# Performance work log

Measured on AMD Instinct MI355X. Metric: run time of the kernel, lower is better.

Reference implementation:

```python
import jax, jax.numpy as jnp
import numpy as np

B, T, C = 4, 128, 512
NH, HS = 8, 64          # n_head, head_dim = C // NH
ORDER = 3               # attention_order
SCALE = 1.0 / np.sqrt(HS)


def setup_inputs() -> dict:
    key = jax.random.key(0)
    ks = jax.random.split(key, 7)
    s = 0.02
    return {
        "x": jax.random.normal(ks[0], (B, T, C), jnp.float32),
        "Wp0": jax.random.normal(ks[1], (C, C), jnp.float32) * s,
        "Wp1": jax.random.normal(ks[2], (C, C), jnp.float32) * s,
        "Wp2": jax.random.normal(ks[3], (C, C), jnp.float32) * s,
        "Wv0": jax.random.normal(ks[4], (HS, HS), jnp.float32) * s,
        "Wv1": jax.random.normal(ks[5], (HS, HS), jnp.float32) * s,
        "Wc": jax.random.normal(ks[6], (C, C), jnp.float32) * s,
    }


def _heads(x, W):
    # Linear then split heads: (B,T,C) -> (B,NH,T,HS)
    return (x @ W).reshape(B, T, NH, HS).transpose(0, 2, 1, 3)


def _causal_mask(t, order):
    # indices grid [T]^order, True where i0 >= i1 >= ... >= i_{order-1}
    idx = jnp.arange(t)
    g = jnp.stack(jnp.meshgrid(*([idx] * order), indexing='ij'), axis=-1)
    return jnp.all(jnp.diff(g, axis=-1) <= 0, axis=-1)


def reference(x, Wp0, Wp1, Wp2, Wv0, Wv1, Wc):
    p0 = _heads(x, Wp0)  # (B,NH,T,HS)
    p1 = _heads(x, Wp1)
    p2 = _heads(x, Wp2)

    # pairwise scores, then higher-order broadcast exactly as the torch einsum
    # ('bh...i,bhkd->bh...ik' sums the key over d and broadcasts — faithful).
    att = jnp.einsum('bhid,bhjd->bhij', p0, p1) * SCALE        # (B,NH,T,T)
    att = jnp.einsum('bh...i,bhkd->bh...ik', att, p2)          # (B,NH,T,T,T)

    mask = _causal_mask(T, ORDER)[None, None]                  # (1,1,T,T,T)
    att = jnp.where(mask, att, -jnp.inf)
    att = jax.nn.softmax(att.reshape(B, NH, T, T * T), axis=-1)

    # value tensors with broadcasted elementwise product over the order dims
    V0 = (p1 @ Wv0)[:, :, :, None, :]   # (B,NH,T,1,HS)
    V1 = (p2 @ Wv1)[:, :, None, :, :]   # (B,NH,1,T,HS)
    V = (V0 * V1).reshape(B, NH, T * T, HS)

    y = jnp.einsum('bhij,bhjd->bhid', att, V)                  # (B,NH,T,HS)
    y = y.transpose(0, 2, 1, 3).reshape(B, T, C)
    return y @ Wc
```

## Files before the change

kernel.cpp:

```cpp
#include <hip/hip_runtime.h>
#include <hip/hip_bf16.h>
#include <math.h>

#define B 4
#define T 128
#define C 512
#define NH 8
#define HS 64
#define BH (B*NH)

typedef __attribute__((ext_vector_type(8))) short bf16x8;
typedef __attribute__((ext_vector_type(4))) float f32x4;

__device__ __forceinline__ unsigned short bfc(float x) {
    return __builtin_bit_cast(unsigned short, __float2bfloat16(x));
}
__device__ __forceinline__ unsigned int pk_bf16(float a, float b) {
    return (unsigned int)bfc(a) | ((unsigned int)bfc(b) << 16);
}
__device__ __forceinline__ float lo_f(unsigned int g) {
    return __builtin_bit_cast(float, g << 16);
}
__device__ __forceinline__ float hi_f(unsigned int g) {
    return __builtin_bit_cast(float, g & 0xffff0000u);
}

__global__ __launch_bounds__(256) void proj_kernel(
    const float* __restrict__ X,
    const float* __restrict__ Wp0, const float* __restrict__ Wp1, const float* __restrict__ Wp2,
    unsigned short* __restrict__ p0b, unsigned short* __restrict__ p1b,
    unsigned short* __restrict__ p2b, float* __restrict__ rr)
{
    __shared__ __align__(16) unsigned short As[32][72];
    __shared__ __align__(16) unsigned short Bs[64][72];
    __shared__ float Ls[64][69];
    __shared__ float sRS[4][32];
    const int z = blockIdx.z;
    const float* W = (z == 0) ? Wp0 : (z == 1) ? Wp1 : Wp2;
    const int m0 = blockIdx.y * 32, n0 = blockIdx.x * 64;
    const int tid = threadIdx.x;
    const int w = tid >> 6, lane = tid & 63, quad = lane >> 4, l16 = lane & 15;
    f32x4 acc[2];
    #pragma unroll
    for (int mt = 0; mt < 2; ++mt) acc[mt] = (f32x4){0.f, 0.f, 0.f, 0.f};

    for (int k0 = 0; k0 < 512; k0 += 64) {
        __syncthreads();
        {
            const int row = tid >> 3, c8 = (tid & 7) * 8;
            const float4 a = *(const float4*)&X[(size_t)(m0 + row) * 512 + k0 + c8];
            const float4 b = *(const float4*)&X[(size_t)(m0 + row) * 512 + k0 + c8 + 4];
            uint4 o;
            o.x = pk_bf16(a.x, a.y);
            o.y = pk_bf16(a.z, a.w);
            o.z = pk_bf16(b.x, b.y);
            o.w = pk_bf16(b.z, b.w);
            *(uint4*)&As[row][c8] = o;
        }
        #pragma unroll
        for (int it = 0; it < 4; ++it) {
            const int q = tid + it * 256;
            const int row = q >> 4, c4 = (q & 15) * 4;
            const float4 v = *(const float4*)&W[(size_t)(k0 + row) * 512 + n0 + c4];
            Ls[row][c4 + 0] = v.x; Ls[row][c4 + 1] = v.y;
            Ls[row][c4 + 2] = v.z; Ls[row][c4 + 3] = v.w;
        }
        __syncthreads();
        #pragma unroll
        for (int it = 0; it < 2; ++it) {
            const int q = tid + it * 256;
            const int nrow = q >> 3, k8 = (q & 7) * 8;
            uint4 o;
            o.x = pk_bf16(Ls[k8 + 0][nrow], Ls[k8 + 1][nrow]);
            o.y = pk_bf16(Ls[k8 + 2][nrow], Ls[k8 + 3][nrow]);
            o.z = pk_bf16(Ls[k8 + 4][nrow], Ls[k8 + 5][nrow]);
            o.w = pk_bf16(Ls[k8 + 6][nrow], Ls[k8 + 7][nrow]);
            *(uint4*)&Bs[nrow][k8] = o;
        }
        __syncthreads();
        #pragma unroll
        for (int kt = 0; kt < 2; ++kt) {
            const bf16x8 b8 = *(const bf16x8*)&Bs[w * 16 + l16][kt * 32 + quad * 8];
            #pragma unroll
            for (int mt = 0; mt < 2; ++mt) {
                const bf16x8 a8 = *(const bf16x8*)&As[mt * 16 + l16][kt * 32 + quad * 8];
                acc[mt] = __builtin_amdgcn_mfma_f32_16x16x32_bf16(a8, b8, acc[mt], 0, 0, 0);
            }
        }
    }

    {
        const int n = n0 + w * 16 + l16;
        const int h = n >> 6, d = n & 63;
        unsigned short* pz = (z == 0) ? p0b : (z == 1) ? p1b : p2b;
        #pragma unroll
        for (int mt = 0; mt < 2; ++mt) {
            #pragma unroll
            for (int r = 0; r < 4; ++r) {
                const int m = m0 + mt * 16 + quad * 4 + r;
                const int bb = m >> 7, t = m & 127;
                pz[((size_t)(bb * NH + h) * T + t) * HS + d] = bfc(acc[mt][r]);
            }
        }
    }
    if (z == 2) {
        #pragma unroll
        for (int mt = 0; mt < 2; ++mt)
            #pragma unroll
            for (int r = 0; r < 4; ++r) {
                float v = acc[mt][r];
                v += __shfl_xor(v, 1, 64); v += __shfl_xor(v, 2, 64);
                v += __shfl_xor(v, 4, 64); v += __shfl_xor(v, 8, 64);
                if (l16 == 0) sRS[w][mt * 16 + quad * 4 + r] = v;
            }
        __syncthreads();
        if (tid < 32) {
            const float s = sRS[0][tid] + sRS[1][tid] + sRS[2][tid] + sRS[3][tid];
            const int m = m0 + tid, bb = m >> 7, tl = m & 127, h = n0 >> 6;
            rr[(bb * NH + h) * T + tl] = s;
        }
    }
}

__global__ __launch_bounds__(512, 4) void attn_kernel(
    const unsigned short* __restrict__ p0b, const unsigned short* __restrict__ p1b,
    const unsigned short* __restrict__ p2b, const float* __restrict__ rr,
    const float* __restrict__ Wv0, const float* __restrict__ Wv1,
    unsigned short* __restrict__ Yb)
{
    __shared__ __align__(16) unsigned short sV0T[64][136];
    __shared__ __align__(16) unsigned short sV1T[64][136];
    __shared__ __align__(16) union {
        unsigned short sWv[64][72];
        float sY[8][8][64];
    } u2;
    __shared__ float sS[8][128];
    __shared__ float srr[128];
    __shared__ float sZarr[8][8];

    const int bid = blockIdx.x;
    const int bh = bid & (BH - 1);
    const int ig = bid >> 5;
    const int tid = threadIdx.x;
    const int w = tid >> 6;
    const int lane = tid & 63;
    const int quad = lane >> 4;
    const int l16 = lane & 15;

    if (tid < 128) srr[tid] = rr[bh * T + tid];

    #pragma unroll
    for (int it = 0; it < 2; ++it) {
        const int k = (tid >> 4) + it * 32;
        const int d0 = (tid & 15) * 4;
        const float4 wv = *(const float4*)&Wv0[(size_t)k * 64 + d0];
        u2.sWv[d0 + 0][k] = bfc(wv.x); u2.sWv[d0 + 1][k] = bfc(wv.y);
        u2.sWv[d0 + 2][k] = bfc(wv.z); u2.sWv[d0 + 3][k] = bfc(wv.w);
    }
    __syncthreads();

    {
        f32x4 vacc[4];
        #pragma unroll
        for (int mt = 0; mt < 4; ++mt) vacc[mt] = (f32x4){0.f, 0.f, 0.f, 0.f};
        #pragma unroll
        for (int kt = 0; kt < 2; ++kt) {
            const bf16x8 b8 = *(const bf16x8*)&p1b[((size_t)bh * T + w * 16 + l16) * HS + kt * 32 + quad * 8];
            #pragma unroll
            for (int mt = 0; mt < 4; ++mt) {
                const bf16x8 a8 = *(const bf16x8*)&u2.sWv[mt * 16 + l16][kt * 32 + quad * 8];
                vacc[mt] = __builtin_amdgcn_mfma_f32_16x16x32_bf16(a8, b8, vacc[mt], 0, 0, 0);
            }
        }
        #pragma unroll
        for (int mt = 0; mt < 4; ++mt)
            #pragma unroll
            for (int r = 0; r < 4; ++r)
                sV0T[mt * 16 + quad * 4 + r][w * 16 + l16] = bfc(vacc[mt][r]);
    }
    __syncthreads();

    #pragma unroll
    for (int it = 0; it < 2; ++it) {
        const int k = (tid >> 4) + it * 32;
        const int d0 = (tid & 15) * 4;
        const float4 wv = *(const float4*)&Wv1[(size_t)k * 64 + d0];
        u2.sWv[d0 + 0][k] = bfc(wv.x); u2.sWv[d0 + 1][k] = bfc(wv.y);
        u2.sWv[d0 + 2][k] = bfc(wv.z); u2.sWv[d0 + 3][k] = bfc(wv.w);
    }
    __syncthreads();

    {
        f32x4 vacc[4];
        #pragma unroll
        for (int mt = 0; mt < 4; ++mt) vacc[mt] = (f32x4){0.f, 0.f, 0.f, 0.f};
        #pragma unroll
        for (int kt = 0; kt < 2; ++kt) {
            const bf16x8 b8 = *(const bf16x8*)&p2b[((size_t)bh * T + w * 16 + l16) * HS + kt * 32 + quad * 8];
            #pragma unroll
            for (int mt = 0; mt < 4; ++mt) {
                const bf16x8 a8 = *(const bf16x8*)&u2.sWv[mt * 16 + l16][kt * 32 + quad * 8];
                vacc[mt] = __builtin_amdgcn_mfma_f32_16x16x32_bf16(a8, b8, vacc[mt], 0, 0, 0);
            }
        }
        #pragma unroll
        for (int mt = 0; mt < 4; ++mt)
            #pragma unroll
            for (int r = 0; r < 4; ++r)
                sV1T[mt * 16 + quad * 4 + r][w * 16 + l16] = bfc(vacc[mt][r]);
    }
    __syncthreads();

    {
        const int qr = l16 & 7;
        const int irow = (qr & 1) ? (16 * qr + 15 - ig) : (16 * qr + ig);
        const unsigned short* ap = p0b + ((size_t)bh * T + irow) * HS + (quad << 3);
        const unsigned short* bp = p1b + (size_t)bh * T * HS + (quad << 3);
        f32x4 s0 = (f32x4){0.f, 0.f, 0.f, 0.f};
        #pragma unroll
        for (int kt = 0; kt < 2; ++kt) {
            const bf16x8 a8 = *(const bf16x8*)(ap + (kt << 5));
            const bf16x8 b0 = *(const bf16x8*)(bp + (size_t)((w << 4) + l16) * HS + (kt << 5));
            s0 = __builtin_amdgcn_mfma_f32_16x16x32_bf16(a8, b0, s0, 0, 0, 0);
        }
        if (quad < 2) {
            #pragma unroll
            for (int r = 0; r < 4; ++r)
                sS[quad * 4 + r][(w << 4) + l16] = s0[r] * 0.125f;
        }
    }
    #pragma unroll
    for (int it = 0; it < 8; ++it) ((float*)u2.sY)[tid + it * 512] = 0.f;
    if (tid < 64) ((float*)sZarr)[tid] = 0.f;
    __syncthreads();

    const float L2E = 1.4426950408889634f;

    float mhat;
    {
        float aS = 0.f;
        #pragma unroll
        for (int q = 0; q < 8; ++q) {
            aS = fmaxf(aS, fabsf(sS[q][lane]));
            aS = fmaxf(aS, fabsf(sS[q][64 + lane]));
        }
        float aR = fmaxf(fabsf(srr[lane]), fabsf(srr[64 + lane]));
        #pragma unroll
        for (int off = 32; off; off >>= 1) {
            aS = fmaxf(aS, __shfl_xor(aS, off, 64));
            aR = fmaxf(aR, __shfl_xor(aR, off, 64));
        }
        mhat = aS * aR;
    }
    const float bexp = -mhat * L2E;
    const int jrow = (w << 4) + l16;
    const int ktmax = w >> 1;

    for (int qq = 7; qq >= w; --qq) {
        const int i = (qq & 1) ? (16 * qq + 15 - ig) : (16 * qq + ig);
        const float aL = sS[qq][jrow] * L2E;
        const bool rowok = (jrow <= i);
        f32x4 acc[4];
        #pragma unroll
        for (int dt = 0; dt < 4; ++dt) acc[dt] = (f32x4){0.f, 0.f, 0.f, 0.f};
        float zacc = 0.f;

        for (int kt = 0; kt <= ktmax; ++kt) {
            const int kbase = (kt << 5) + (quad << 3);
            float rk[8];
            *(float4*)&rk[0] = *(const float4*)&srr[kbase];
            *(float4*)&rk[4] = *(const float4*)&srr[kbase + 4];
            const int dlim = rowok ? (jrow - kbase) : -1;
            float e[8];
            #pragma unroll
            for (int q = 0; q < 8; ++q) {
                const float ex = __builtin_amdgcn_exp2f(fmaf(aL, rk[q], bexp));
                e[q] = (q <= dlim) ? ex : 0.f;
                zacc += e[q];
            }
            uint4 o;
            o.x = pk_bf16(e[0], e[1]);
            o.y = pk_bf16(e[2], e[3]);
            o.z = pk_bf16(e[4], e[5]);
            o.w = pk_bf16(e[6], e[7]);
            const bf16x8 a8 = __builtin_bit_cast(bf16x8, o);
            #pragma unroll
            for (int dt = 0; dt < 4; ++dt) {
                const bf16x8 b8 = *(const bf16x8*)&sV1T[(dt << 4) + l16][(quad << 3) + (kt << 5)];
                acc[dt] = __builtin_amdgcn_mfma_f32_16x16x32_bf16(a8, b8, acc[dt], 0, 0, 0);
            }
        }

        float part[4];
        #pragma unroll
        for (int dt = 0; dt < 4; ++dt) {
            const uint2 uu = *(const uint2*)&sV0T[(dt << 4) + l16][(w << 4) + (quad << 2)];
            float p = 0.f;
            if (w < qq) {
                p = fmaf(lo_f(uu.x), acc[dt][0], p);
                p = fmaf(hi_f(uu.x), acc[dt][1], p);
                p = fmaf(lo_f(uu.y), acc[dt][2], p);
                p = fmaf(hi_f(uu.y), acc[dt][3], p);
            } else {
                const int jb = (w << 4) + (quad << 2);
                if (jb + 0 <= i) p = fmaf(lo_f(uu.x), acc[dt][0], p);
                if (jb + 1 <= i) p = fmaf(hi_f(uu.x), acc[dt][1], p);
                if (jb + 2 <= i) p = fmaf(lo_f(uu.y), acc[dt][2], p);
                if (jb + 3 <= i) p = fmaf(hi_f(uu.y), acc[dt][3], p);
            }
            p += __shfl_xor(p, 16, 64);
            p += __shfl_xor(p, 32, 64);
            part[dt] = p;
        }
        const float sel = (quad == 0) ? part[0] : (quad == 1) ? part[1] : (quad == 2) ? part[2] : part[3];
        u2.sY[qq][w][lane] = sel;

        #pragma unroll
        for (int off = 32; off; off >>= 1) zacc += __shfl_xor(zacc, off, 64);
        if (lane == 0) sZarr[qq][w] = zacc;
    }
    __syncthreads();

    {
        const int qq = w;
        const int i = (qq & 1) ? (16 * qq + 15 - ig) : (16 * qq + ig);
        float Z = 0.f;
        #pragma unroll
        for (int ww = 0; ww < 8; ++ww) Z += sZarr[qq][ww];
        float y = 0.f;
        #pragma unroll
        for (int ww = 0; ww < 8; ++ww) y += u2.sY[qq][ww][lane];
        const int bb = bh >> 3, hh = bh & 7;
        Yb[((size_t)(bb * T + i) * C) + hh * HS + lane] = bfc(y / Z);
    }
}

__global__ __launch_bounds__(256) void outmm_kernel(
    const unsigned short* __restrict__ Ab, const float* __restrict__ Wc,
    float* __restrict__ OUT)
{
    __shared__ __align__(16) unsigned short As[32][72];
    __shared__ __align__(16) unsigned short Bs[64][72];
    __shared__ float Ls[64][69];
    const int m0 = blockIdx.y * 32, n0 = blockIdx.x * 64;
    const int tid = threadIdx.x;
    const int w = tid >> 6, lane = tid & 63, quad = lane >> 4, l16 = lane & 15;
    f32x4 acc[2];
    #pragma unroll
    for (int mt = 0; mt < 2; ++mt) acc[mt] = (f32x4){0.f, 0.f, 0.f, 0.f};
    for (int k0 = 0; k0 < 512; k0 += 64) {
        __syncthreads();
        {
            const int row = tid >> 3, c8 = (tid & 7) * 8;
            *(uint4*)&As[row][c8] = *(const uint4*)&Ab[(size_t)(m0 + row) * 512 + k0 + c8];
        }
        #pragma unroll
        for (int it = 0; it < 4; ++it) {
            const int q = tid + it * 256;
            const int row = q >> 4, c4 = (q & 15) * 4;
            const float4 v = *(const float4*)&Wc[(size_t)(k0 + row) * 512 + n0 + c4];
            Ls[row][c4 + 0] = v.x; Ls[row][c4 + 1] = v.y;
            Ls[row][c4 + 2] = v.z; Ls[row][c4 + 3] = v.w;
        }
        __syncthreads();
        #pragma unroll
        for (int it = 0; it < 2; ++it) {
            const int q = tid + it * 256;
            const int nrow = q >> 3, k8 = (q & 7) * 8;
            uint4 o;
            o.x = pk_bf16(Ls[k8 + 0][nrow], Ls[k8 + 1][nrow]);
            o.y = pk_bf16(Ls[k8 + 2][nrow], Ls[k8 + 3][nrow]);
            o.z = pk_bf16(Ls[k8 + 4][nrow], Ls[k8 + 5][nrow]);
            o.w = pk_bf16(Ls[k8 + 6][nrow], Ls[k8 + 7][nrow]);
            *(uint4*)&Bs[nrow][k8] = o;
        }
        __syncthreads();
        #pragma unroll
        for (int kt = 0; kt < 2; ++kt) {
            const bf16x8 b8 = *(const bf16x8*)&Bs[w * 16 + l16][kt * 32 + quad * 8];
            #pragma unroll
            for (int mt = 0; mt < 2; ++mt) {
                const bf16x8 a8 = *(const bf16x8*)&As[mt * 16 + l16][kt * 32 + quad * 8];
                acc[mt] = __builtin_amdgcn_mfma_f32_16x16x32_bf16(a8, b8, acc[mt], 0, 0, 0);
            }
        }
    }
    const int n = n0 + w * 16 + l16;
    #pragma unroll
    for (int mt = 0; mt < 2; ++mt)
        #pragma unroll
        for (int r = 0; r < 4; ++r) {
            const int mrow = m0 + mt * 16 + quad * 4 + r;
            OUT[(size_t)mrow * 512 + n] = acc[mt][r];
        }
}

extern "C" void kernel_launch(void* const* d_in, const int* in_sizes, int n_in,
                              void* d_out, int out_size, void* d_ws, size_t ws_size,
                              hipStream_t stream)
{
    const float* x   = (const float*)d_in[0];
    const float* Wp0 = (const float*)d_in[1];
    const float* Wp1 = (const float*)d_in[2];
    const float* Wp2 = (const float*)d_in[3];
    const float* Wv0 = (const float*)d_in[4];
    const float* Wv1 = (const float*)d_in[5];
    const float* Wc  = (const float*)d_in[6];
    float* out = (float*)d_out;

    char* w8 = (char*)d_ws;
    const size_t HB = 512 * 1024;
    unsigned short* p0b = (unsigned short*)(w8 + 0 * HB);
    unsigned short* p1b = (unsigned short*)(w8 + 1 * HB);
    unsigned short* p2b = (unsigned short*)(w8 + 2 * HB);
    unsigned short* Yb  = (unsigned short*)(w8 + 3 * HB);
    float*          rr  = (float*)        (w8 + 4 * HB);

    proj_kernel <<<dim3(8, 16, 3), 256, 0, stream>>>(x, Wp0, Wp1, Wp2, p0b, p1b, p2b, rr);
    attn_kernel <<<dim3(512), 512, 0, stream>>>(p0b, p1b, p2b, rr, Wv0, Wv1, Yb);
    outmm_kernel<<<dim3(8, 16), 256, 0, stream>>>(Yb, Wc, out);
}
```

Measured before the change: 104.0 us.

## Fuse value projections into projection kernel and store transposed V tiles

Computes V0 = p1@Wv0 and V1 = p2@Wv1 in the epilogue of proj_kernel while the projection tile is still in registers, and writes them to global memory already transposed in bf16. The attention kernel then loads ready-made V0T/V1T tiles instead of converting Wv and running two small MFMA passes plus several barriers. Before, each of the 512 attention blocks redundantly recomputed the per-head V matrices (16 blocks per head). The cost is a longer proj_kernel epilogue, extra global traffic for the V tensors, and p2b is no longer written.

```diff
diff --git a/kernel.cpp b/kernel.cpp
--- a/kernel.cpp
+++ b/kernel.cpp
@@ -28,8 +28,10 @@
 __global__ __launch_bounds__(256) void proj_kernel(
     const float* __restrict__ X,
     const float* __restrict__ Wp0, const float* __restrict__ Wp1, const float* __restrict__ Wp2,
+    const float* __restrict__ Wv0, const float* __restrict__ Wv1,
     unsigned short* __restrict__ p0b, unsigned short* __restrict__ p1b,
-    unsigned short* __restrict__ p2b, float* __restrict__ rr)
+    unsigned short* __restrict__ V0T, unsigned short* __restrict__ V1T,
+    float* __restrict__ rr)
 {
     __shared__ __align__(16) unsigned short As[32][72];
     __shared__ __align__(16) unsigned short Bs[64][72];
@@ -89,10 +91,10 @@
         }
     }
 
-    {
+    if (z != 2) {
         const int n = n0 + w * 16 + l16;
         const int h = n >> 6, d = n & 63;
-        unsigned short* pz = (z == 0) ? p0b : (z == 1) ? p1b : p2b;
+        unsigned short* pz = (z == 0) ? p0b : p1b;
         #pragma unroll
         for (int mt = 0; mt < 2; ++mt) {
             #pragma unroll
@@ -120,23 +122,63 @@
             rr[(bb * NH + h) * T + tl] = s;
         }
     }
+
+    if (z >= 1) {
+        const float* Wv = (z == 1) ? Wv0 : Wv1;
+        unsigned short* VT = (z == 1) ? V0T : V1T;
+        __syncthreads();
+        #pragma unroll
+        for (int mt = 0; mt < 2; ++mt)
+            #pragma unroll
+            for (int r = 0; r < 4; ++r)
+                As[mt * 16 + quad * 4 + r][w * 16 + l16] = bfc(acc[mt][r]);
+        #pragma unroll
+        for (int it = 0; it < 4; ++it) {
+            const int k = (tid >> 4) + it * 16;
+            const int d0 = (tid & 15) * 4;
+            const float4 wv = *(const float4*)&Wv[(size_t)k * 64 + d0];
+            Bs[d0 + 0][k] = bfc(wv.x); Bs[d0 + 1][k] = bfc(wv.y);
+            Bs[d0 + 2][k] = bfc(wv.z); Bs[d0 + 3][k] = bfc(wv.w);
+        }
+        __syncthreads();
+        f32x4 vacc[2];
+        #pragma unroll
+        for (int mt = 0; mt < 2; ++mt) vacc[mt] = (f32x4){0.f, 0.f, 0.f, 0.f};
+        #pragma unroll
+        for (int kt = 0; kt < 2; ++kt) {
+            const bf16x8 b8 = *(const bf16x8*)&Bs[w * 16 + l16][kt * 32 + quad * 8];
+            #pragma unroll
+            for (int mt = 0; mt < 2; ++mt) {
+                const bf16x8 a8 = *(const bf16x8*)&As[mt * 16 + l16][kt * 32 + quad * 8];
+                vacc[mt] = __builtin_amdgcn_mfma_f32_16x16x32_bf16(a8, b8, vacc[mt], 0, 0, 0);
+            }
+        }
+        const int h = n0 >> 6;
+        const int bb = m0 >> 7, t0 = m0 & 127;
+        const int bh = bb * NH + h;
+        const int dp = w * 16 + l16;
+        #pragma unroll
+        for (int mt = 0; mt < 2; ++mt) {
+            uint2 o;
+            o.x = pk_bf16(vacc[mt][0], vacc[mt][1]);
+            o.y = pk_bf16(vacc[mt][2], vacc[mt][3]);
+            *(uint2*)&VT[((size_t)bh * HS + dp) * T + t0 + mt * 16 + quad * 4] = o;
+        }
+    }
 }
 
 __global__ __launch_bounds__(512, 4) void attn_kernel(
     const unsigned short* __restrict__ p0b, const unsigned short* __restrict__ p1b,
-    const unsigned short* __restrict__ p2b, const float* __restrict__ rr,
-    const float* __restrict__ Wv0, const float* __restrict__ Wv1,
+    const float* __restrict__ rr,
+    const unsigned short* __restrict__ V0Tg, const unsigned short* __restrict__ V1Tg,
     unsigned short* __restrict__ Yb)
 {
     __shared__ __align__(16) unsigned short sV0T[64][136];
     __shared__ __align__(16) unsigned short sV1T[64][136];
-    __shared__ __align__(16) union {
-        unsigned short sWv[64][72];
-        float sY[8][8][64];
-    } u2;
     __shared__ float sS[8][128];
     __shared__ float srr[128];
     __shared__ float sZarr[8][8];
+    __shared__ float sY[8][8][64];
 
     const int bid = blockIdx.x;
     const int bh = bid & (BH - 1);
@@ -151,65 +193,11 @@
 
     #pragma unroll
     for (int it = 0; it < 2; ++it) {
-        const int k = (tid >> 4) + it * 32;
-        const int d0 = (tid & 15) * 4;
-        const float4 wv = *(const float4*)&Wv0[(size_t)k * 64 + d0];
-        u2.sWv[d0 + 0][k] = bfc(wv.x); u2.sWv[d0 + 1][k] = bfc(wv.y);
-        u2.sWv[d0 + 2][k] = bfc(wv.z); u2.sWv[d0 + 3][k] = bfc(wv.w);
-    }
-    __syncthreads();
-
-    {
-        f32x4 vacc[4];
-        #pragma unroll
-        for (int mt = 0; mt < 4; ++mt) vacc[mt] = (f32x4){0.f, 0.f, 0.f, 0.f};
-        #pragma unroll
-        for (int kt = 0; kt < 2; ++kt) {
-            const bf16x8 b8 = *(const bf16x8*)&p1b[((size_t)bh * T + w * 16 + l16) * HS + kt * 32 + quad * 8];
-            #pragma unroll
-            for (int mt = 0; mt < 4; ++mt) {
-                const bf16x8 a8 = *(const bf16x8*)&u2.sWv[mt * 16 + l16][kt * 32 + quad * 8];
-                vacc[mt] = __builtin_amdgcn_mfma_f32_16x16x32_bf16(a8, b8, vacc[mt], 0, 0, 0);
-            }
-        }
-        #pragma unroll
-        for (int mt = 0; mt < 4; ++mt)
-            #pragma unroll
-            for (int r = 0; r < 4; ++r)
-                sV0T[mt * 16 + quad * 4 + r][w * 16 + l16] = bfc(vacc[mt][r]);
-    }
-    __syncthreads();
-
-    #pragma unroll
-    for (int it = 0; it < 2; ++it) {
-        const int k = (tid >> 4) + it * 32;
-        const int d0 = (tid & 15) * 4;
-        const float4 wv = *(const float4*)&Wv1[(size_t)k * 64 + d0];
-        u2.sWv[d0 + 0][k] = bfc(wv.x); u2.sWv[d0 + 1][k] = bfc(wv.y);
-        u2.sWv[d0 + 2][k] = bfc(wv.z); u2.sWv[d0 + 3][k] = bfc(wv.w);
-    }
-    __syncthreads();
-
-    {
-        f32x4 vacc[4];
-        #pragma unroll
-        for (int mt = 0; mt < 4; ++mt) vacc[mt] = (f32x4){0.f, 0.f, 0.f, 0.f};
-        #pragma unroll
-        for (int kt = 0; kt < 2; ++kt) {
-            const bf16x8 b8 = *(const bf16x8*)&p2b[((size_t)bh * T + w * 16 + l16) * HS + kt * 32 + quad * 8];
-            #pragma unroll
-            for (int mt = 0; mt < 4; ++mt) {
-                const bf16x8 a8 = *(const bf16x8*)&u2.sWv[mt * 16 + l16][kt * 32 + quad * 8];
-                vacc[mt] = __builtin_amdgcn_mfma_f32_16x16x32_bf16(a8, b8, vacc[mt], 0, 0, 0);
-            }
-        }
-        #pragma unroll
-        for (int mt = 0; mt < 4; ++mt)
-            #pragma unroll
-            for (int r = 0; r < 4; ++r)
-                sV1T[mt * 16 + quad * 4 + r][w * 16 + l16] = bfc(vacc[mt][r]);
-    }
-    __syncthreads();
+        const int q = tid + it * 512;
+        const int row = q >> 4, c8 = (q & 15) * 8;
+        *(uint4*)&sV0T[row][c8] = *(const uint4*)&V0Tg[((size_t)bh * HS + row) * T + c8];
+        *(uint4*)&sV1T[row][c8] = *(const uint4*)&V1Tg[((size_t)bh * HS + row) * T + c8];
+    }
 
     {
         const int qr = l16 & 7;
@@ -230,7 +218,7 @@
         }
     }
     #pragma unroll
-    for (int it = 0; it < 8; ++it) ((float*)u2.sY)[tid + it * 512] = 0.f;
+    for (int it = 0; it < 8; ++it) ((float*)sY)[tid + it * 512] = 0.f;
     if (tid < 64) ((float*)sZarr)[tid] = 0.f;
     __syncthreads();
 
@@ -313,7 +301,7 @@
             part[dt] = p;
         }
         const float sel = (quad == 0) ? part[0] : (quad == 1) ? part[1] : (quad == 2) ? part[2] : part[3];
-        u2.sY[qq][w][lane] = sel;
+        sY[qq][w][lane] = sel;
 
         #pragma unroll
         for (int off = 32; off; off >>= 1) zacc += __shfl_xor(zacc, off, 64);
@@ -329,7 +317,7 @@
         for (int ww = 0; ww < 8; ++ww) Z += sZarr[qq][ww];
         float y = 0.f;
         #pragma unroll
-        for (int ww = 0; ww < 8; ++ww) y += u2.sY[qq][ww][lane];
+        for (int ww = 0; ww < 8; ++ww) y += sY[qq][ww][lane];
         const int bb = bh >> 3, hh = bh & 7;
         Yb[((size_t)(bb * T + i) * C) + hh * HS + lane] = bfc(y / Z);
     }
@@ -412,11 +400,13 @@
     const size_t HB = 512 * 1024;
     unsigned short* p0b = (unsigned short*)(w8 + 0 * HB);
     unsigned short* p1b = (unsigned short*)(w8 + 1 * HB);
-    unsigned short* p2b = (unsigned short*)(w8 + 2 * HB);
-    unsigned short* Yb  = (unsigned short*)(w8 + 3 * HB);
-    float*          rr  = (float*)        (w8 + 4 * HB);
-
-    proj_kernel <<<dim3(8, 16, 3), 256, 0, stream>>>(x, Wp0, Wp1, Wp2, p0b, p1b, p2b, rr);
-    attn_kernel <<<dim3(512), 512, 0, stream>>>(p0b, p1b, p2b, rr, Wv0, Wv1, Yb);
+    unsigned short* V0T = (unsigned short*)(w8 + 2 * HB);
+    unsigned short* V1T = (unsigned short*)(w8 + 3 * HB);
+    unsigned short* Yb  = (unsigned short*)(w8 + 4 * HB);
+    float*          rr  = (float*)        (w8 + 5 * HB);
+
+    proj_kernel <<<dim3(8, 16, 3), 256, 0, stream>>>(x, Wp0, Wp1, Wp2, Wv0, Wv1,
+                                                     p0b, p1b, V0T, V1T, rr);
+    attn_kernel <<<dim3(512), 512, 0, stream>>>(p0b, p1b, rr, V0T, V1T, Yb);
     outmm_kernel<<<dim3(8, 16), 256, 0, stream>>>(Yb, Wc, out);
 }
```

After: 100.5 us, median of 2. 1.03x faster.
